# Kernel tuning notes

Hardware: AMD Instinct MI355X
Metric: run time of the kernel (lower is better)

The kernel has to match this reference:

```python
import jax, jax.numpy as jnp
import numpy as np

B, S, D = 32, 4096, 256


def setup_inputs() -> dict:
    key = jax.random.key(0)
    k1, k2, k3, k4 = jax.random.split(key, 4)
    return {
        "wM": jax.random.normal(k1, (B, S, D), dtype=jnp.float32),
        "wd": jax.random.normal(k2, (B, S, D), dtype=jnp.float32),
        "e1": jax.random.normal(k3, (B, D), dtype=jnp.float32),
        "e2": jax.random.normal(k4, (B, D), dtype=jnp.float32),
    }


def reference(wM, wd, e1, e2):
    # Entity-attention scores: per-position dot of wd[b,s,:] with entity embedding e[b,:].
    # (The original repeats e over S and batch_dots along the feature axis.)
    A1 = jnp.einsum("bsd,bd->bs", wd, e1)  # [B,S]
    A2 = jnp.einsum("bsd,bd->bs", wd, e2)  # [B,S]
    alpha1 = jax.nn.softmax(A1, axis=-1)
    alpha2 = jax.nn.softmax(A2, axis=-1)
    alpha = (alpha1 ** 2 + alpha2 ** 2) * 0.5  # [B,S]
    return wM * alpha[..., None]  # [B,S,D]
```

## Files before the change

### kernel.cpp

```cpp
#include <hip/hip_runtime.h>

#define BB 32
#define SS 4096
#define DD 256
#define RD 8
#define RS 4
#define PW (SS / RD)
#define CSHIFT 40.0f

typedef float f4v __attribute__((ext_vector_type(4)));

__global__ __launch_bounds__(256) void dots_kernel(const float* __restrict__ wd,
                                                   const float* __restrict__ e1,
                                                   const float* __restrict__ e2,
                                                   float* __restrict__ A1,
                                                   float* __restrict__ A2,
                                                   float* __restrict__ psumA,
                                                   float* __restrict__ psumB) {
    const int wave = (int)((blockIdx.x * blockDim.x + threadIdx.x) >> 6);
    const int lane = threadIdx.x & 63;
    const int row0 = wave * RD;
    const int b = row0 >> 12;

    const f4v* e1v = reinterpret_cast<const f4v*>(e1 + b * DD);
    const f4v* e2v = reinterpret_cast<const f4v*>(e2 + b * DD);
    const f4v x1 = e1v[lane];
    const f4v x2 = e2v[lane];

    const f4v* wdv = reinterpret_cast<const f4v*>(wd) + (size_t)row0 * (DD / 4) + lane;
    f4v w[RD];
    #pragma unroll
    for (int r = 0; r < RD; ++r) w[r] = __builtin_nontemporal_load(&wdv[r * (DD / 4)]);

    float d1[RD], d2[RD];
    #pragma unroll
    for (int r = 0; r < RD; ++r) {
        d1[r] = w[r].x * x1.x + w[r].y * x1.y + w[r].z * x1.z + w[r].w * x1.w;
        d2[r] = w[r].x * x2.x + w[r].y * x2.y + w[r].z * x2.z + w[r].w * x2.w;
    }
    #pragma unroll
    for (int m = 32; m >= 1; m >>= 1) {
        #pragma unroll
        for (int r = 0; r < RD; ++r) {
            d1[r] += __shfl_xor(d1[r], m, 64);
            d2[r] += __shfl_xor(d2[r], m, 64);
        }
    }
    if (lane == 0) {
        float p = 0.0f;
        #pragma unroll
        for (int r = 0; r < RD; ++r) {
            A1[row0 + r] = d1[r];
            p += __expf(d1[r] - CSHIFT);
        }
        psumA[wave] = p;
    }
    if (lane == 1) {
        float p = 0.0f;
        #pragma unroll
        for (int r = 0; r < RD; ++r) {
            A2[row0 + r] = d2[r];
            p += __expf(d2[r] - CSHIFT);
        }
        psumB[wave] = p;
    }
}

__global__ __launch_bounds__(256) void scale_kernel(const float* __restrict__ wM,
                                                    const float* __restrict__ A1,
                                                    const float* __restrict__ A2,
                                                    const float* __restrict__ psumA,
                                                    const float* __restrict__ psumB,
                                                    float* __restrict__ out) {
    const int wave = (int)((blockIdx.x * blockDim.x + threadIdx.x) >> 6);
    const int lane = threadIdx.x & 63;
    const int row0 = wave * RS;
    const int b = row0 >> 12;

    const f4v* in = reinterpret_cast<const f4v*>(wM) + (size_t)row0 * (DD / 4) + lane;
    f4v* o = reinterpret_cast<f4v*>(out) + (size_t)row0 * (DD / 4) + lane;
    f4v v[RS];
    #pragma unroll
    for (int r = 0; r < RS; ++r) v[r] = __builtin_nontemporal_load(&in[r * (DD / 4)]);

    const float* pA = psumA + b * PW;
    const float* pB = psumB + b * PW;
    float l1 = 0.0f, l2 = 0.0f;
    #pragma unroll
    for (int k = 0; k < PW / 64; ++k) {
        l1 += pA[lane + k * 64];
        l2 += pB[lane + k * 64];
    }
    #pragma unroll
    for (int m = 32; m >= 1; m >>= 1) {
        l1 += __shfl_xor(l1, m, 64);
        l2 += __shfl_xor(l2, m, 64);
    }
    const float il1 = 1.0f / l1;
    const float il2 = 1.0f / l2;

    float alpha[RS];
    #pragma unroll
    for (int r = 0; r < RS; ++r) {
        const float a1 = __expf(A1[row0 + r] - CSHIFT) * il1;
        const float a2 = __expf(A2[row0 + r] - CSHIFT) * il2;
        alpha[r] = 0.5f * (a1 * a1 + a2 * a2);
    }

    #pragma unroll
    for (int r = 0; r < RS; ++r) {
        f4v vv = v[r];
        vv.x *= alpha[r]; vv.y *= alpha[r]; vv.z *= alpha[r]; vv.w *= alpha[r];
        __builtin_nontemporal_store(vv, &o[r * (DD / 4)]);
    }
}

extern "C" void kernel_launch(void* const* d_in, const int* in_sizes, int n_in,
                              void* d_out, int out_size, void* d_ws, size_t ws_size,
                              hipStream_t stream) {
    const float* wM = (const float*)d_in[0];
    const float* wd = (const float*)d_in[1];
    const float* e1 = (const float*)d_in[2];
    const float* e2 = (const float*)d_in[3];
    float* out = (float*)d_out;

    float* A1 = (float*)d_ws;
    float* A2 = A1 + (size_t)BB * SS;
    float* psumA = A2 + (size_t)BB * SS;
    float* psumB = psumA + (size_t)BB * PW;

    const int rows = BB * SS;
    dots_kernel<<<rows / (4 * RD), 256, 0, stream>>>(wd, e1, e2, A1, A2, psumA, psumB);
    scale_kernel<<<rows / (4 * RS), 256, 0, stream>>>(wM, A1, A2, psumA, psumB, out);
}
```

Baseline: 70.42 us.

## Fuse dots and scale kernels into one cooperative persistent kernel with grid sync

Replaces the two-kernel launch with a single cooperative persistent kernel. Each wave first computes the dot products and partial exp-sums for a contiguous chunk of rows, then all waves meet at a grid-wide sync, and afterwards each wave scales the wM rows of its chunk. The goal is to remove the second kernel launch and the gap between the two kernels. The cost is a grid barrier, fewer resident waves with serial per-wave loops (which may reduce memory-level parallelism), and a cooperative-launch query on every call. The old two-kernel path is kept as a fallback.

```diff
diff --git a/kernel.cpp b/kernel.cpp
--- a/kernel.cpp
+++ b/kernel.cpp
@@ -1,14 +1,119 @@
 #include <hip/hip_runtime.h>
+#include <hip/hip_cooperative_groups.h>
+
+namespace cg = cooperative_groups;
 
 #define BB 32
 #define SS 4096
 #define DD 256
 #define RD 8
 #define RS 4
+#define ROWS (BB * SS)
 #define PW (SS / RD)
 #define CSHIFT 40.0f
 
 typedef float f4v __attribute__((ext_vector_type(4)));
+
+__global__ __launch_bounds__(256, 4) void fused_kernel(
+        const float* __restrict__ wM,
+        const float* __restrict__ wd,
+        const float* __restrict__ e1,
+        const float* __restrict__ e2,
+        float* __restrict__ A1,
+        float* __restrict__ A2,
+        float* __restrict__ psumA,
+        float* __restrict__ psumB,
+        float* __restrict__ out,
+        int chunk) {
+    const int W = (int)(blockIdx.x * 4 + (threadIdx.x >> 6));
+    const int lane = threadIdx.x & 63;
+    const int rbase = W * chunk;
+    const int b = rbase >> 12;
+
+    const f4v x1 = reinterpret_cast<const f4v*>(e1 + b * DD)[lane];
+    const f4v x2 = reinterpret_cast<const f4v*>(e2 + b * DD)[lane];
+
+    for (int t = 0; t < chunk / RD; ++t) {
+        const int row0 = rbase + t * RD;
+        const f4v* wdv = reinterpret_cast<const f4v*>(wd) + (size_t)row0 * (DD / 4) + lane;
+        f4v w[RD];
+        #pragma unroll
+        for (int r = 0; r < RD; ++r) w[r] = __builtin_nontemporal_load(&wdv[r * (DD / 4)]);
+
+        float d1[RD], d2[RD];
+        #pragma unroll
+        for (int r = 0; r < RD; ++r) {
+            d1[r] = w[r].x * x1.x + w[r].y * x1.y + w[r].z * x1.z + w[r].w * x1.w;
+            d2[r] = w[r].x * x2.x + w[r].y * x2.y + w[r].z * x2.z + w[r].w * x2.w;
+        }
+        #pragma unroll
+        for (int m = 32; m >= 1; m >>= 1) {
+            #pragma unroll
+            for (int r = 0; r < RD; ++r) {
+                d1[r] += __shfl_xor(d1[r], m, 64);
+                d2[r] += __shfl_xor(d2[r], m, 64);
+            }
+        }
+        if (lane == 0) {
+            float p = 0.0f;
+            #pragma unroll
+            for (int r = 0; r < RD; ++r) {
+                A1[row0 + r] = d1[r];
+                p += __expf(d1[r] - CSHIFT);
+            }
+            psumA[row0 / RD] = p;
+        }
+        if (lane == 1) {
+            float p = 0.0f;
+            #pragma unroll
+            for (int r = 0; r < RD; ++r) {
+                A2[row0 + r] = d2[r];
+                p += __expf(d2[r] - CSHIFT);
+            }
+            psumB[row0 / RD] = p;
+        }
+    }
+
+    __threadfence();
+    cg::this_grid().sync();
+
+    float l1 = 0.0f, l2 = 0.0f;
+    #pragma unroll
+    for (int k = 0; k < PW / 64; ++k) {
+        l1 += psumA[b * PW + lane + k * 64];
+        l2 += psumB[b * PW + lane + k * 64];
+    }
+    #pragma unroll
+    for (int m = 32; m >= 1; m >>= 1) {
+        l1 += __shfl_xor(l1, m, 64);
+        l2 += __shfl_xor(l2, m, 64);
+    }
+    const float il1 = 1.0f / l1;
+    const float il2 = 1.0f / l2;
+
+    for (int t = 0; t < chunk / RS; ++t) {
+        const int row0 = rbase + t * RS;
+        const f4v* in = reinterpret_cast<const f4v*>(wM) + (size_t)row0 * (DD / 4) + lane;
+        f4v* o = reinterpret_cast<f4v*>(out) + (size_t)row0 * (DD / 4) + lane;
+        f4v v[RS];
+        #pragma unroll
+        for (int r = 0; r < RS; ++r) v[r] = __builtin_nontemporal_load(&in[r * (DD / 4)]);
+
+        float alpha[RS];
+        #pragma unroll
+        for (int r = 0; r < RS; ++r) {
+            const float a1 = __expf(A1[row0 + r] - CSHIFT) * il1;
+            const float a2 = __expf(A2[row0 + r] - CSHIFT) * il2;
+            alpha[r] = 0.5f * (a1 * a1 + a2 * a2);
+        }
+        #pragma unroll
+        for (int r = 0; r < RS; ++r) {
+            f4v vv = v[r];
+            vv.x *= alpha[r]; vv.y *= alpha[r]; vv.z *= alpha[r]; vv.w *= alpha[r];
+            __builtin_nontemporal_store(vv, &o[r * (DD / 4)]);
+        }
+    }
+}
 
 __global__ __launch_bounds__(256) void dots_kernel(const float* __restrict__ wd,
                                                    const float* __restrict__ e1,
@@ -22,10 +127,8 @@
     const int row0 = wave * RD;
     const int b = row0 >> 12;
 
-    const f4v* e1v = reinterpret_cast<const f4v*>(e1 + b * DD);
-    const f4v* e2v = reinterpret_cast<const f4v*>(e2 + b * DD);
-    const f4v x1 = e1v[lane];
-    const f4v x2 = e2v[lane];
+    const f4v x1 = reinterpret_cast<const f4v*>(e1 + b * DD)[lane];
+    const f4v x2 = reinterpret_cast<const f4v*>(e2 + b * DD)[lane];
 
     const f4v* wdv = reinterpret_cast<const f4v*>(wd) + (size_t)row0 * (DD / 4) + lane;
     f4v w[RD];
@@ -53,7 +156,7 @@
             A1[row0 + r] = d1[r];
             p += __expf(d1[r] - CSHIFT);
         }
-        psumA[wave] = p;
+        psumA[row0 / RD] = p;
     }
     if (lane == 1) {
         float p = 0.0f;
@@ -62,7 +165,7 @@
             A2[row0 + r] = d2[r];
             p += __expf(d2[r] - CSHIFT);
         }
-        psumB[wave] = p;
+        psumB[row0 / RD] = p;
     }
 }
 
@@ -83,13 +186,11 @@
     #pragma unroll
     for (int r = 0; r < RS; ++r) v[r] = __builtin_nontemporal_load(&in[r * (DD / 4)]);
 
-    const float* pA = psumA + b * PW;
-    const float* pB = psumB + b * PW;
     float l1 = 0.0f, l2 = 0.0f;
     #pragma unroll
     for (int k = 0; k < PW / 64; ++k) {
-        l1 += pA[lane + k * 64];
-        l2 += pB[lane + k * 64];
+        l1 += psumA[b * PW + lane + k * 64];
+        l2 += psumB[b * PW + lane + k * 64];
     }
     #pragma unroll
     for (int m = 32; m >= 1; m >>= 1) {
@@ -106,7 +207,6 @@
         const float a2 = __expf(A2[row0 + r] - CSHIFT) * il2;
         alpha[r] = 0.5f * (a1 * a1 + a2 * a2);
     }
-
     #pragma unroll
     for (int r = 0; r < RS; ++r) {
         f4v vv = v[r];
@@ -129,7 +229,29 @@
     float* psumA = A2 + (size_t)BB * SS;
     float* psumB = psumA + (size_t)BB * PW;
 
-    const int rows = BB * SS;
-    dots_kernel<<<rows / (4 * RD), 256, 0, stream>>>(wd, e1, e2, A1, A2, psumA, psumB);
-    scale_kernel<<<rows / (4 * RS), 256, 0, stream>>>(wM, A1, A2, psumA, psumB, out);
-}
+    int blocksPerCU = 0;
+    hipError_t qerr = hipOccupancyMaxActiveBlocksPerMultiprocessor(
+        &blocksPerCU, (const void*)fused_kernel, 256, 0);
+
+    bool coop_ok = false;
+    if (qerr == hipSuccess && blocksPerCU >= 1) {
+        int nblk = blocksPerCU * 256;
+        int p2 = 256;
+        while (p2 * 2 <= nblk && p2 * 2 <= 1024) p2 *= 2;
+        const int nwaves = p2 * 4;
+        const int chunk = ROWS / nwaves;
+
+        void* args[] = {(void*)&wM, (void*)&wd, (void*)&e1, (void*)&e2,
+                        (void*)&A1, (void*)&A2, (void*)&psumA, (void*)&psumB,
+                        (void*)&out, (void*)&chunk};
+        hipError_t lerr = hipLaunchCooperativeKernel((const void*)fused_kernel,
+                                                     dim3(p2), dim3(256),
+                                                     args, 0, stream);
+        coop_ok = (lerr == hipSuccess);
+    }
+
+    if (!coop_ok) {
+        dots_kernel<<<ROWS / (4 * RD), 256, 0, stream>>>(wd, e1, e2, A1, A2, psumA, psumB);
+        scale_kernel<<<ROWS / (4 * RS), 256, 0, stream>>>(wM, A1, A2, psumA, psumB, out);
+    }
+}
```

Result: slower. 209.0 us (+196.8%).
